# Kernel tuning notes

Measured on AMD Instinct MI355X. Metric: run time of the kernel, lower is better.

The kernel has to match this reference:

```python
import jax, jax.numpy as jnp
import numpy as np

EPS = 1e-6
COEF_CLIP = 120.0
ACTIVE_IDX = 0


def setup_inputs() -> dict:
    key = jax.random.key(0)
    ks = jax.random.split(key, 7)
    A, T, H = 4, 8192, 2048
    return {
        "hidden_states": jax.random.normal(ks[0], (A, T, H), dtype=jnp.float32),
        "activated": jax.random.normal(ks[1], (T, H), dtype=jnp.float32),
        "router_norm_weight": jax.random.uniform(ks[2], (H,), dtype=jnp.float32),
        "w_router": jax.random.normal(ks[3], (A, H), dtype=jnp.float32),
        "w_pred": jax.random.normal(ks[4], (A * A, A), dtype=jnp.float32),
        "w_corr": jax.random.normal(ks[5], (A, A), dtype=jnp.float32),
        "correct_output_scale": jax.random.normal(ks[6], (H,), dtype=jnp.float32),
    }


def reference(hidden_states, activated, router_norm_weight, w_router, w_pred,
              w_corr, correct_output_scale):
    A, T, H = hidden_states.shape
    router_input_scale = 1.0 / H

    def rmsnorm(x):
        xf = x.astype(jnp.float32)
        var = jnp.mean(xf * xf, axis=-1, keepdims=True)
        return (xf * jax.lax.rsqrt(var + EPS)) * router_norm_weight

    def modalities(x):
        # [T, H] -> [T, A]
        r = rmsnorm(x) * router_input_scale
        return jnp.tanh(r @ w_router.T)

    # ---- predict ----
    m_pred = modalities(hidden_states[ACTIVE_IDX])                 # [T, A]
    wp = jnp.clip(w_pred, -COEF_CLIP, COEF_CLIP)                   # [A*A, A]
    # reshape [T, A, A] then permute(0, 2, 1)
    all_coefs = (m_pred @ wp.T).reshape(T, A, A).transpose(0, 2, 1)
    # matmul(hs.permute(1,2,0)[T,H,A], all_coefs[T,A,B]) -> permute(2,0,1) -> [B,T,H]
    predictions = jnp.einsum('ath,tab->bth', hidden_states, all_coefs)
    predictions = predictions + hidden_states                      # [A, T, H]

    # ---- correct ----
    m_corr = modalities(activated)                                 # [T, A]
    wc = jnp.clip(w_corr, -COEF_CLIP, COEF_CLIP)                   # [A, A]
    cc = (m_corr @ wc.T) + 1.0                                     # [T, A]
    innovation = activated - predictions[ACTIVE_IDX]               # [T, H]
    corrected = innovation[None, :, :] * cc.T[:, :, None] + predictions  # [A,T,H]

    # ---- scale active output ----
    output = corrected[ACTIVE_IDX] * correct_output_scale          # [T, H]
    return corrected, output
```

## Files before the change

### kernel.cpp

```cpp
#include <hip/hip_runtime.h>
#include <math.h>

namespace {

typedef float f32x4 __attribute__((ext_vector_type(4)));

constexpr int A = 4;
constexpr int H = 2048;
constexpr int BLK = 512;
constexpr float EPSV = 1e-6f;
constexpr float CLIPV = 120.0f;

__device__ __forceinline__ float clipv(float v) {
    return fminf(fmaxf(v, -CLIPV), CLIPV);
}

__global__ __launch_bounds__(BLK, 4) void altup_fused(
    const float* __restrict__ hs,
    const float* __restrict__ act,
    const float* __restrict__ rnw,
    const float* __restrict__ w_router,
    const float* __restrict__ w_pred,
    const float* __restrict__ w_corr,
    const float* __restrict__ oscale,
    float* __restrict__ out,
    int T)
{
    const int t   = blockIdx.x;
    const int tid = threadIdx.x;
    const size_t TH = (size_t)T * H;
    const size_t rowOff = (size_t)t * H;
    const int h = tid * 4;

    const f32x4 x0 = __builtin_nontemporal_load((const f32x4*)(hs + rowOff + h));
    const f32x4 av = __builtin_nontemporal_load((const f32x4*)(act + rowOff + h));
    const f32x4 x1 = __builtin_nontemporal_load((const f32x4*)(hs + 1 * TH + rowOff + h));
    const f32x4 x2 = __builtin_nontemporal_load((const f32x4*)(hs + 2 * TH + rowOff + h));
    const f32x4 x3 = __builtin_nontemporal_load((const f32x4*)(hs + 3 * TH + rowOff + h));
    const f32x4 rv = *(const f32x4*)(rnw + h);
    const f32x4 sv = *(const f32x4*)(oscale + h);
    const f32x4 w0 = *(const f32x4*)(w_router + 0 * H + h);
    const f32x4 w1 = *(const f32x4*)(w_router + 1 * H + h);
    const f32x4 w2 = *(const f32x4*)(w_router + 2 * H + h);
    const f32x4 w3 = *(const f32x4*)(w_router + 3 * H + h);

    float part[10];
#pragma unroll
    for (int i = 0; i < 10; ++i) part[i] = 0.f;
#pragma unroll
    for (int k = 0; k < 4; ++k) {
        const float x = x0[k], a = av[k], r = rv[k];
        part[0] = fmaf(x, x, part[0]);
        part[5] = fmaf(a, a, part[5]);
        const float xr = x * r;
        const float ar = a * r;
        part[1] = fmaf(xr, w0[k], part[1]);
        part[2] = fmaf(xr, w1[k], part[2]);
        part[3] = fmaf(xr, w2[k], part[3]);
        part[4] = fmaf(xr, w3[k], part[4]);
        part[6] = fmaf(ar, w0[k], part[6]);
        part[7] = fmaf(ar, w1[k], part[7]);
        part[8] = fmaf(ar, w2[k], part[8]);
        part[9] = fmaf(ar, w3[k], part[9]);
    }

#pragma unroll
    for (int off = 32; off >= 1; off >>= 1) {
#pragma unroll
        for (int i = 0; i < 10; ++i) part[i] += __shfl_down(part[i], off, 64);
    }

    __shared__ float red[10][8];
    const int wave = tid >> 6;
    const int lane = tid & 63;
    if (lane == 0) {
#pragma unroll
        for (int i = 0; i < 10; ++i) red[i][wave] = part[i];
    }
    __syncthreads();

    float sums[10];
#pragma unroll
    for (int i = 0; i < 10; ++i) {
        const f32x4 lo = *(const f32x4*)&red[i][0];
        const f32x4 hi = *(const f32x4*)&red[i][4];
        sums[i] = ((lo[0] + lo[1]) + (lo[2] + lo[3])) +
                  ((hi[0] + hi[1]) + (hi[2] + hi[3]));
    }

    const float invH = 1.0f / (float)H;
    const float sp = rsqrtf(sums[0] * invH + EPSV) * invH;
    const float sc = rsqrtf(sums[5] * invH + EPSV) * invH;
    float mp[4], mc[4];
#pragma unroll
    for (int j = 0; j < 4; ++j) {
        mp[j] = tanhf(sums[1 + j] * sp);
        mc[j] = tanhf(sums[6 + j] * sc);
    }

    float coef[4][4];
#pragma unroll
    for (int b = 0; b < 4; ++b) {
#pragma unroll
        for (int a = 0; a < 4; ++a) {
            float s = 0.f;
#pragma unroll
            for (int j = 0; j < 4; ++j)
                s = fmaf(mp[j], clipv(w_pred[(b * 4 + a) * A + j]), s);
            coef[a][b] = s;
        }
    }
    float cc[4];
#pragma unroll
    for (int a = 0; a < 4; ++a) {
        float s = 1.0f;
#pragma unroll
        for (int j = 0; j < 4; ++j)
            s = fmaf(mc[j], clipv(w_corr[a * A + j]), s);
        cc[a] = s;
    }

    f32x4 co[4], ov;
#pragma unroll
    for (int k = 0; k < 4; ++k) {
        const float xs4[4] = {x0[k], x1[k], x2[k], x3[k]};
        float pr[4];
#pragma unroll
        for (int b = 0; b < 4; ++b) {
            float s = xs4[b];
#pragma unroll
            for (int a = 0; a < 4; ++a)
                s = fmaf(xs4[a], coef[a][b], s);
            pr[b] = s;
        }
        const float innov = av[k] - pr[0];
#pragma unroll
        for (int a = 0; a < 4; ++a)
            co[a][k] = fmaf(innov, cc[a], pr[a]);
        ov[k] = co[0][k] * sv[k];
    }
#pragma unroll
    for (int a = 0; a < 4; ++a)
        __builtin_nontemporal_store(co[a], (f32x4*)(out + (size_t)a * TH + rowOff + h));
    __builtin_nontemporal_store(ov, (f32x4*)(out + (size_t)A * TH + rowOff + h));
}

}

extern "C" void kernel_launch(void* const* d_in, const int* in_sizes, int n_in,
                              void* d_out, int out_size, void* d_ws, size_t ws_size,
                              hipStream_t stream) {
    const float* hs       = (const float*)d_in[0];
    const float* act      = (const float*)d_in[1];
    const float* rnw      = (const float*)d_in[2];
    const float* w_router = (const float*)d_in[3];
    const float* w_pred   = (const float*)d_in[4];
    const float* w_corr   = (const float*)d_in[5];
    const float* oscale   = (const float*)d_in[6];
    float* out = (float*)d_out;

    const int T = in_sizes[1] / H;

    altup_fused<<<dim3(T), dim3(BLK), 0, stream>>>(
        hs, act, rnw, w_router, w_pred, w_corr, oscale, out, T);
}
```

Baseline: 134.6 us.

## Map one wavefront per token row to drop block-level reduction and barrier

Each 64-lane wavefront now handles a whole token row of 2048 elements across 8 chunks, so the reductions become wave-level xor shuffles with no shared memory or __syncthreads. The row and activated vectors stay in registers between the two phases, while hidden-state slices 1-3 are loaded only in the second phase, chunk by chunk, which shrinks the set of values live at once. Blocks shrink to 256 threads covering 4 rows. The cost is more registers per lane for the 16 kept vectors and longer serial work per wave, which could lower occupancy or the number of memory requests in flight.

```diff
diff --git a/kernel.cpp b/kernel.cpp
--- a/kernel.cpp
+++ b/kernel.cpp
@@ -7,7 +7,7 @@
 
 constexpr int A = 4;
 constexpr int H = 2048;
-constexpr int BLK = 512;
+constexpr int BLK = 256;
 constexpr float EPSV = 1e-6f;
 constexpr float CLIPV = 120.0f;
 
@@ -15,7 +15,7 @@
     return fminf(fmaxf(v, -CLIPV), CLIPV);
 }
 
-__global__ __launch_bounds__(BLK, 4) void altup_fused(
+__global__ __launch_bounds__(BLK) void altup_wave(
     const float* __restrict__ hs,
     const float* __restrict__ act,
     const float* __restrict__ rnw,
@@ -26,81 +26,65 @@
     float* __restrict__ out,
     int T)
 {
-    const int t   = blockIdx.x;
-    const int tid = threadIdx.x;
+    const int tid  = threadIdx.x;
+    const int wave = tid >> 6;
+    const int lane = tid & 63;
+    const int t    = blockIdx.x * (BLK / 64) + wave;
     const size_t TH = (size_t)T * H;
-    const size_t rowOff = (size_t)t * H;
-    const int h = tid * 4;
+    const size_t ro = (size_t)t * H;
 
-    const f32x4 x0 = __builtin_nontemporal_load((const f32x4*)(hs + rowOff + h));
-    const f32x4 av = __builtin_nontemporal_load((const f32x4*)(act + rowOff + h));
-    const f32x4 x1 = __builtin_nontemporal_load((const f32x4*)(hs + 1 * TH + rowOff + h));
-    const f32x4 x2 = __builtin_nontemporal_load((const f32x4*)(hs + 2 * TH + rowOff + h));
-    const f32x4 x3 = __builtin_nontemporal_load((const f32x4*)(hs + 3 * TH + rowOff + h));
-    const f32x4 rv = *(const f32x4*)(rnw + h);
-    const f32x4 sv = *(const f32x4*)(oscale + h);
-    const f32x4 w0 = *(const f32x4*)(w_router + 0 * H + h);
-    const f32x4 w1 = *(const f32x4*)(w_router + 1 * H + h);
-    const f32x4 w2 = *(const f32x4*)(w_router + 2 * H + h);
-    const f32x4 w3 = *(const f32x4*)(w_router + 3 * H + h);
-
+    f32x4 x0[8], av[8];
     float part[10];
 #pragma unroll
-    for (int i = 0; i < 10; ++i) part[i] = 0.f;
+    for (int q = 0; q < 10; ++q) part[q] = 0.f;
+
 #pragma unroll
-    for (int k = 0; k < 4; ++k) {
-        const float x = x0[k], a = av[k], r = rv[k];
-        part[0] = fmaf(x, x, part[0]);
-        part[5] = fmaf(a, a, part[5]);
-        const float xr = x * r;
-        const float ar = a * r;
-        part[1] = fmaf(xr, w0[k], part[1]);
-        part[2] = fmaf(xr, w1[k], part[2]);
-        part[3] = fmaf(xr, w2[k], part[3]);
-        part[4] = fmaf(xr, w3[k], part[4]);
-        part[6] = fmaf(ar, w0[k], part[6]);
-        part[7] = fmaf(ar, w1[k], part[7]);
-        part[8] = fmaf(ar, w2[k], part[8]);
-        part[9] = fmaf(ar, w3[k], part[9]);
+    for (int c = 0; c < 8; ++c) {
+        const int h = c * 256 + lane * 4;
+        x0[c] = __builtin_nontemporal_load((const f32x4*)(hs + ro + h));
+        av[c] = __builtin_nontemporal_load((const f32x4*)(act + ro + h));
+        const f32x4 r  = *(const f32x4*)(rnw + h);
+        const f32x4 w0 = *(const f32x4*)(w_router + 0 * H + h);
+        const f32x4 w1 = *(const f32x4*)(w_router + 1 * H + h);
+        const f32x4 w2 = *(const f32x4*)(w_router + 2 * H + h);
+        const f32x4 w3 = *(const f32x4*)(w_router + 3 * H + h);
+#pragma unroll
+        for (int k = 0; k < 4; ++k) {
+            const float x = x0[c][k], a = av[c][k], rr = r[k];
+            part[0] = fmaf(x, x, part[0]);
+            part[5] = fmaf(a, a, part[5]);
+            const float xr = x * rr;
+            const float ar = a * rr;
+            part[1] = fmaf(xr, w0[k], part[1]);
+            part[2] = fmaf(xr, w1[k], part[2]);
+            part[3] = fmaf(xr, w2[k], part[3]);
+            part[4] = fmaf(xr, w3[k], part[4]);
+            part[6] = fmaf(ar, w0[k], part[6]);
+            part[7] = fmaf(ar, w1[k], part[7]);
+            part[8] = fmaf(ar, w2[k], part[8]);
+            part[9] = fmaf(ar, w3[k], part[9]);
+        }
     }
 
 #pragma unroll
     for (int off = 32; off >= 1; off >>= 1) {
 #pragma unroll
-        for (int i = 0; i < 10; ++i) part[i] += __shfl_down(part[i], off, 64);
-    }
-
-    __shared__ float red[10][8];
-    const int wave = tid >> 6;
-    const int lane = tid & 63;
-    if (lane == 0) {
-#pragma unroll
-        for (int i = 0; i < 10; ++i) red[i][wave] = part[i];
-    }
-    __syncthreads();
-
-    float sums[10];
-#pragma unroll
-    for (int i = 0; i < 10; ++i) {
-        const f32x4 lo = *(const f32x4*)&red[i][0];
-        const f32x4 hi = *(const f32x4*)&red[i][4];
-        sums[i] = ((lo[0] + lo[1]) + (lo[2] + lo[3])) +
-                  ((hi[0] + hi[1]) + (hi[2] + hi[3]));
+        for (int q = 0; q < 10; ++q) part[q] += __shfl_xor(part[q], off, 64);
     }
 
     const float invH = 1.0f / (float)H;
-    const float sp = rsqrtf(sums[0] * invH + EPSV) * invH;
-    const float sc = rsqrtf(sums[5] * invH + EPSV) * invH;
+    const float sp = rsqrtf(part[0] * invH + EPSV) * invH;
+    const float sc = rsqrtf(part[5] * invH + EPSV) * invH;
     float mp[4], mc[4];
 #pragma unroll
     for (int j = 0; j < 4; ++j) {
-        mp[j] = tanhf(sums[1 + j] * sp);
-        mc[j] = tanhf(sums[6 + j] * sc);
+        mp[j] = tanhf(part[1 + j] * sp);
+        mc[j] = tanhf(part[6 + j] * sc);
     }
 
     float coef[4][4];
 #pragma unroll
-    for (int b = 0; b < 4; ++b) {
+    for (int b = 0; b < 4; ++b)
 #pragma unroll
         for (int a = 0; a < 4; ++a) {
             float s = 0.f;
@@ -109,7 +93,6 @@
                 s = fmaf(mp[j], clipv(w_pred[(b * 4 + a) * A + j]), s);
             coef[a][b] = s;
         }
-    }
     float cc[4];
 #pragma unroll
     for (int a = 0; a < 4; ++a) {
@@ -120,29 +103,40 @@
         cc[a] = s;
     }
 
-    f32x4 co[4], ov;
 #pragma unroll
-    for (int k = 0; k < 4; ++k) {
-        const float xs4[4] = {x0[k], x1[k], x2[k], x3[k]};
-        float pr[4];
+    for (int c = 0; c < 8; ++c) {
+        const int h = c * 256 + lane * 4;
+        const f32x4 x1 = __builtin_nontemporal_load((const f32x4*)(hs + 1 * TH + ro + h));
+        const f32x4 x2 = __builtin_nontemporal_load((const f32x4*)(hs + 2 * TH + ro + h));
+        const f32x4 x3 = __builtin_nontemporal_load((const f32x4*)(hs + 3 * TH + ro + h));
+        const f32x4 sv = *(const f32x4*)(oscale + h);
+
+        f32x4 co0, co1, co2, co3, ov;
 #pragma unroll
-        for (int b = 0; b < 4; ++b) {
-            float s = xs4[b];
+        for (int k = 0; k < 4; ++k) {
+            const float xs4[4] = {x0[c][k], x1[k], x2[k], x3[k]};
+            float pr[4];
 #pragma unroll
-            for (int a = 0; a < 4; ++a)
-                s = fmaf(xs4[a], coef[a][b], s);
-            pr[b] = s;
+            for (int b = 0; b < 4; ++b) {
+                float s = xs4[b];
+#pragma unroll
+                for (int a = 0; a < 4; ++a)
+                    s = fmaf(xs4[a], coef[a][b], s);
+                pr[b] = s;
+            }
+            const float innov = av[c][k] - pr[0];
+            co0[k] = fmaf(innov, cc[0], pr[0]);
+            co1[k] = fmaf(innov, cc[1], pr[1]);
+            co2[k] = fmaf(innov, cc[2], pr[2]);
+            co3[k] = fmaf(innov, cc[3], pr[3]);
+            ov[k]  = co0[k] * sv[k];
         }
-        const float innov = av[k] - pr[0];
-#pragma unroll
-        for (int a = 0; a < 4; ++a)
-            co[a][k] = fmaf(innov, cc[a], pr[a]);
-        ov[k] = co[0][k] * sv[k];
+        __builtin_nontemporal_store(co0, (f32x4*)(out + 0 * TH + ro + h));
+        __builtin_nontemporal_store(co1, (f32x4*)(out + 1 * TH + ro + h));
+        __builtin_nontemporal_store(co2, (f32x4*)(out + 2 * TH + ro + h));
+        __builtin_nontemporal_store(co3, (f32x4*)(out + 3 * TH + ro + h));
+        __builtin_nontemporal_store(ov,  (f32x4*)(out + (size_t)A * TH + ro + h));
     }
-#pragma unroll
-    for (int a = 0; a < 4; ++a)
-        __builtin_nontemporal_store(co[a], (f32x4*)(out + (size_t)a * TH + rowOff + h));
-    __builtin_nontemporal_store(ov, (f32x4*)(out + (size_t)A * TH + rowOff + h));
 }
 
 }
@@ -160,7 +154,8 @@
     float* out = (float*)d_out;
 
     const int T = in_sizes[1] / H;
+    const int G = T / (BLK / 64);
 
-    altup_fused<<<dim3(T), dim3(BLK), 0, stream>>>(
+    altup_wave<<<dim3(G), dim3(BLK), 0, stream>>>(
         hs, act, rnw, w_router, w_pred, w_corr, oscale, out, T);
 }
```

New measurement: 161.2 us. 1.2x slower.
